# Performance work log

Hardware: AMD Instinct MI355X
Metric: run time of the kernel (lower is better)

The kernel has to match this reference:

```python
import jax, jax.numpy as jnp
import numpy as np

CTX, H, ENC, BALL = 256, 128, 128, 2
IN_DIM = 2 + BALL + ENC  # prev_disp(2) + ball(2) + encoding(128)
B, T = 8192, 128


def setup_inputs() -> dict:
    key = jax.random.key(0)
    ks = jax.random.split(key, 16)
    s = lambda fan_in: 1.0 / np.sqrt(fan_in)
    inp = {
        "context": jax.random.normal(ks[0], (B, CTX), jnp.float32),
        "target_encoding": jax.random.normal(ks[1], (B, ENC), jnp.float32),
        "ball_land_xy": jax.random.normal(ks[2], (B, BALL), jnp.float32),
        "max_frames": T,
        # context_to_h / context_to_c
        "Wh": jax.random.uniform(ks[3], (H, CTX), jnp.float32, -s(CTX), s(CTX)),
        "bh": jax.random.uniform(ks[4], (H,), jnp.float32, -s(CTX), s(CTX)),
        "Wc": jax.random.uniform(ks[5], (H, CTX), jnp.float32, -s(CTX), s(CTX)),
        "bc": jax.random.uniform(ks[6], (H,), jnp.float32, -s(CTX), s(CTX)),
        # LSTM (PyTorch gate order: i, f, g, o)
        "W_ih": jax.random.uniform(ks[7], (4 * H, IN_DIM), jnp.float32, -s(H), s(H)),
        "W_hh": jax.random.uniform(ks[8], (4 * H, H), jnp.float32, -s(H), s(H)),
        "b_ih": jax.random.uniform(ks[9], (4 * H,), jnp.float32, -s(H), s(H)),
        "b_hh": jax.random.uniform(ks[10], (4 * H,), jnp.float32, -s(H), s(H)),
        # output head
        "Wo": jax.random.uniform(ks[11], (2, H), jnp.float32, -s(H), s(H)),
        "bo": jax.random.uniform(ks[12], (2,), jnp.float32, -s(H), s(H)),
    }
    return inp


def _decode(context, target_encoding, ball_land_xy, Wh, bh, Wc, bc,
            W_ih, W_hh, b_ih, b_hh, Wo, bo, max_frames):
    h0 = context @ Wh.T + bh                      # (B, H)
    c0 = context @ Wc.T + bc                      # (B, H)
    Bn = context.shape[0]
    # split input weights: first 2 cols act on prev_disp, rest on static [ball, enc]
    W_prev = W_ih[:, :2]                          # (4H, 2)
    W_stat = W_ih[:, 2:]                          # (4H, BALL+ENC)
    static_in = jnp.concatenate([ball_land_xy, target_encoding], axis=-1)
    gate_static = static_in @ W_stat.T + b_ih + b_hh  # (B, 4H), constant per step
    Hn = h0.shape[-1]

    def step(carry, _):
        h, c, prev = carry
        gates = prev @ W_prev.T + h @ W_hh.T + gate_static
        i, f, g, o = jnp.split(gates, 4, axis=-1)
        c = jax.nn.sigmoid(f) * c + jax.nn.sigmoid(i) * jnp.tanh(g)
        h = jax.nn.sigmoid(o) * jnp.tanh(c)
        pred = h @ Wo.T + bo                      # (B, 2)
        prev = jax.lax.stop_gradient(pred)        # matches .detach()
        return (h, c, prev), pred

    prev0 = jnp.zeros((Bn, 2), dtype=context.dtype)
    _, preds = jax.lax.scan(step, (h0, c0, prev0), None, length=max_frames)
    return jnp.transpose(preds, (1, 0, 2))        # (B, T, 2)


def reference(context, target_encoding, ball_land_xy, max_frames,
              Wh, bh, Wc, bc, W_ih, W_hh, b_ih, b_hh, Wo, bo):
    return _decode(context, target_encoding, ball_land_xy, Wh, bh, Wc, bc,
                   W_ih, W_hh, b_ih, b_hh, Wo, bo, max_frames)
```

## Files before the change

kernel.cpp:

```cpp
#include <hip/hip_runtime.h>
#include <hip/hip_bf16.h>


#define HDIM 128
#define CTX_DIM 256
#define T_FRAMES 128
#define BB 16
#define STR 136

typedef __bf16 bf16x8 __attribute__((ext_vector_type(8)));
typedef float  f32x4  __attribute__((ext_vector_type(4)));

union frag_u {
  bf16x8 v;
  unsigned short s[8];
  uint4 u4;
};

#if __has_builtin(__builtin_amdgcn_exp2f)
#define EXP2(x) __builtin_amdgcn_exp2f(x)
#else
#define EXP2(x) __expf((x) * 0.6931471805599453f)
#endif
#define RCP(x) __builtin_amdgcn_rcpf(x)

__device__ __forceinline__ unsigned short f2bf(float x) {
  unsigned u = __builtin_bit_cast(unsigned, x);
  u += 0x7FFFu + ((u >> 16) & 1u);
  return (unsigned short)(u >> 16);
}
__device__ __forceinline__ float bf2f(unsigned short h) {
  unsigned u = ((unsigned)h) << 16;
  return __builtin_bit_cast(float, u);
}
template<int CTRL>
__device__ __forceinline__ float dpp_mov(float x) {
  return __builtin_bit_cast(float,
    __builtin_amdgcn_mov_dpp(__builtin_bit_cast(int, x), CTRL, 0xF, 0xF, true));
}
__device__ __forceinline__ float row_reduce16(float v) {
  v += dpp_mov<0xB1>(v);
  v += dpp_mov<0x4E>(v);
  v += dpp_mov<0x124>(v);
  v += dpp_mov<0x128>(v);
  return v;
}

#define MFMA(a, b, c) __builtin_amdgcn_mfma_f32_16x16x32_bf16((a), (b), (c), 0, 0, 0)

__global__ __launch_bounds__(512, 4) void traj_lstm(
    const float* __restrict__ ctx, const float* __restrict__ enc,
    const float* __restrict__ ball,
    const float* __restrict__ Wh, const float* __restrict__ bh,
    const float* __restrict__ Wc, const float* __restrict__ bc,
    const float* __restrict__ W_ih, const float* __restrict__ W_hh,
    const float* __restrict__ b_ih, const float* __restrict__ b_hh,
    const float* __restrict__ Wo, const float* __restrict__ bo,
    float* __restrict__ outp)
{
  __shared__ __align__(16) __bf16 sh_h[2][BB * STR];
  __shared__ __align__(16) unsigned short sh_sA[BB * 264];
  __shared__ __align__(16) unsigned short sh_sB[BB * 264];
  __shared__ __align__(16) float sh_gs[4 * HDIM * 16];
  __shared__ __align__(16) uint4 sh_wof[4 * 64];
  __shared__ float sh_pw0[8][BB * 2];
  __shared__ float sh_p0[BB * 2];

  const int tid  = threadIdx.x;
  const int w    = tid >> 6;
  const int l    = tid & 63;
  const int q    = l >> 4;
  const int c16  = l & 15;
  const int colH = w * 16 + c16;
  const int rbase = blockIdx.x * BB;

  const float Lc = 1.4426950408889634f;
  const float SG[4] = {Lc, Lc, 2.f * Lc, Lc};
  const float bo0 = bo[0], bo1 = bo[1];
  const float wo0 = Wo[colH], wo1 = Wo[HDIM + colH];

  float wp0[4], wp1[4];
  #pragma unroll
  for (int g = 0; g < 4; ++g) {
    wp0[g] = W_ih[(size_t)(g * HDIM + colH) * 132 + 0];
    wp1[g] = W_ih[(size_t)(g * HDIM + colH) * 132 + 1];
  }

  frag_u Wf[4][4];
  #pragma unroll
  for (int kt = 0; kt < 4; ++kt) {
    const float* w0p = Wo + kt * 32 + q * 8;
    const float* w1p = Wo + HDIM + kt * 32 + q * 8;
    float4 a0 = *(const float4*)w0p, a1 = *(const float4*)(w0p + 4);
    float4 b0 = *(const float4*)w1p, b1 = *(const float4*)(w1p + 4);
    float wo0v[8] = {a0.x, a0.y, a0.z, a0.w, a1.x, a1.y, a1.z, a1.w};
    float wo1v[8] = {b0.x, b0.y, b0.z, b0.w, b1.x, b1.y, b1.z, b1.w};
    #pragma unroll
    for (int g = 0; g < 4; ++g) {
      const float* wr = W_hh + (size_t)(g * HDIM + colH) * HDIM + kt * 32 + q * 8;
      float4 f0 = *(const float4*)wr;
      float4 f1 = *(const float4*)(wr + 4);
      float ff[8] = {f0.x, f0.y, f0.z, f0.w, f1.x, f1.y, f1.z, f1.w};
      #pragma unroll
      for (int j = 0; j < 8; ++j)
        Wf[g][kt].s[j] = f2bf(SG[g] * (ff[j] + wp0[g] * wo0v[j] + wp1[g] * wo1v[j]));
    }
  }

  #pragma unroll
  for (int kt = 0; kt < 4; ++kt) {
    frag_u wf;
    #pragma unroll
    for (int j = 0; j < 8; ++j) {
      float x = (c16 < 2) ? Wo[c16 * HDIM + kt * 32 + q * 8 + j] : 0.f;
      wf.s[j] = f2bf(x);
    }
    if (w == 0) sh_wof[kt * 64 + l] = wf.u4;
  }

  for (int e = tid; e < BB * 256; e += 512) {
    int row = e >> 8, col = e & 255;
    float x = ctx[(size_t)(rbase + row) * CTX_DIM + col];
    unsigned short hb = f2bf(x);
    sh_sA[row * 264 + col] = hb;
    sh_sB[row * 264 + col] = f2bf(x - bf2f(hb));
  }
  __syncthreads();

  float cst[4];
  {
    f32x4 aH = {0.f,0.f,0.f,0.f};
    f32x4 aC = {0.f,0.f,0.f,0.f};
    #pragma unroll
    for (int kt = 0; kt < 8; ++kt) {
      frag_u Ahi, Alo;
      Ahi.u4 = *(const uint4*)&sh_sA[c16 * 264 + kt * 32 + q * 8];
      Alo.u4 = *(const uint4*)&sh_sB[c16 * 264 + kt * 32 + q * 8];
      frag_u bhi, blo;
      {
        const float* wr = Wh + (size_t)colH * CTX_DIM + kt * 32 + q * 8;
        float4 f0 = *(const float4*)wr;
        float4 f1 = *(const float4*)(wr + 4);
        float ff[8] = {f0.x, f0.y, f0.z, f0.w, f1.x, f1.y, f1.z, f1.w};
        #pragma unroll
        for (int j = 0; j < 8; ++j) {
          unsigned short hb = f2bf(ff[j]);
          bhi.s[j] = hb;
          blo.s[j] = f2bf(ff[j] - bf2f(hb));
        }
      }
      aH = MFMA(Ahi.v, bhi.v, aH);
      aH = MFMA(Alo.v, bhi.v, aH);
      aH = MFMA(Ahi.v, blo.v, aH);
      {
        const float* wr = Wc + (size_t)colH * CTX_DIM + kt * 32 + q * 8;
        float4 f0 = *(const float4*)wr;
        float4 f1 = *(const float4*)(wr + 4);
        float ff[8] = {f0.x, f0.y, f0.z, f0.w, f1.x, f1.y, f1.z, f1.w};
        #pragma unroll
        for (int j = 0; j < 8; ++j) {
          unsigned short hb = f2bf(ff[j]);
          bhi.s[j] = hb;
          blo.s[j] = f2bf(ff[j] - bf2f(hb));
        }
      }
      aC = MFMA(Ahi.v, bhi.v, aC);
      aC = MFMA(Alo.v, bhi.v, aC);
      aC = MFMA(Ahi.v, blo.v, aC);
    }
    float bhv = bh[colH], bcv = bc[colH];
    float pp0[4][2];
    #pragma unroll
    for (int r = 0; r < 4; ++r) {
      float h0v = aH[r] + bhv;
      cst[r] = aC[r] + bcv;
      sh_h[0][(q * 4 + r) * STR + colH] = (__bf16)h0v;
      pp0[r][0] = h0v * wo0;
      pp0[r][1] = h0v * wo1;
    }
    #pragma unroll
    for (int m = 0; m < 4; ++m) {
      pp0[m][0] = row_reduce16(pp0[m][0]);
      pp0[m][1] = row_reduce16(pp0[m][1]);
    }
    if (c16 == 0) {
      #pragma unroll
      for (int r = 0; r < 4; ++r) {
        sh_pw0[w][(q * 4 + r) * 2 + 0] = pp0[r][0];
        sh_pw0[w][(q * 4 + r) * 2 + 1] = pp0[r][1];
      }
    }
  }
  __syncthreads();

  for (int e = tid; e < BB * 168; e += 512) {
    int row = e / 168, col = e - row * 168;
    float x = (col < 2) ? ball[(size_t)(rbase + row) * 2 + col]
            : (col < 130) ? enc[(size_t)(rbase + row) * 128 + (col - 2)] : 0.f;
    unsigned short hb = f2bf(x);
    sh_sA[row * 168 + col] = hb;
    sh_sB[row * 168 + col] = f2bf(x - bf2f(hb));
  }
  if (tid < BB * 2) {
    float s = (tid & 1) ? bo1 : bo0;
    #pragma unroll
    for (int w2 = 0; w2 < 8; ++w2) s += sh_pw0[w2][tid];
    sh_p0[tid] = s;
  }
  __syncthreads();

  {
    f32x4 gacc[4] = {{0.f,0.f,0.f,0.f},{0.f,0.f,0.f,0.f},
                     {0.f,0.f,0.f,0.f},{0.f,0.f,0.f,0.f}};
    #pragma unroll
    for (int kt = 0; kt < 5; ++kt) {
      frag_u Ahi, Alo;
      Ahi.u4 = *(const uint4*)&sh_sA[c16 * 168 + kt * 32 + q * 8];
      Alo.u4 = *(const uint4*)&sh_sB[c16 * 168 + kt * 32 + q * 8];
      #pragma unroll
      for (int g = 0; g < 4; ++g) {
        frag_u bhi, blo;
        #pragma unroll
        for (int j = 0; j < 8; ++j) {
          int kk = kt * 32 + q * 8 + j;
          float x = (kk < 130) ? SG[g] * W_ih[(size_t)(g * HDIM + colH) * 132 + 2 + kk] : 0.f;
          unsigned short hb = f2bf(x);
          bhi.s[j] = hb;
          blo.s[j] = f2bf(x - bf2f(hb));
        }
        gacc[g] = MFMA(Ahi.v, bhi.v, gacc[g]);
        gacc[g] = MFMA(Alo.v, bhi.v, gacc[g]);
        gacc[g] = MFMA(Ahi.v, blo.v, gacc[g]);
      }
    }
    #pragma unroll
    for (int g = 0; g < 4; ++g) {
      int colG = g * HDIM + colH;
      float bb = SG[g] * (b_ih[colG] + b_hh[colG] + bo0 * wp0[g] + bo1 * wp1[g]);
      f32x4 t = gacc[g];
      t[0] += bb; t[1] += bb; t[2] += bb; t[3] += bb;
      *(f32x4*)&sh_gs[((g * HDIM + colH) * 4 + q) * 4] = t;
    }
  }
  float wps0[4], wps1[4];
  #pragma unroll
  for (int g = 0; g < 4; ++g) {
    wps0[g] = SG[g] * wp0[g];
    wps1[g] = SG[g] * wp1[g];
  }

  auto body = [&](int t, int rbuf, bool first) {
    const int wbuf = rbuf ^ 1;
    const __bf16* hp = &sh_h[rbuf][c16 * STR];

    f32x4 acc[4];
    #pragma unroll
    for (int g = 0; g < 4; ++g)
      acc[g] = *(const f32x4*)&sh_gs[((g * HDIM + colH) * 4 + q) * 4];
    f32x4 accP = {0.f, 0.f, 0.f, 0.f};

    #pragma unroll
    for (int kt = 0; kt < 4; ++kt) {
      frag_u A;
      A.u4 = *(const uint4*)(hp + kt * 32 + q * 8);
      #pragma unroll
      for (int g = 0; g < 4; ++g)
        acc[g] = MFMA(A.v, Wf[g][kt].v, acc[g]);
      if (!first && w == 7) {
        frag_u wof;
        wof.u4 = sh_wof[kt * 64 + l];
        accP = MFMA(A.v, wof.v, accP);
      }
    }
    if (first) {
      #pragma unroll
      for (int r = 0; r < 4; ++r) {
        float2 p0r = *(const float2*)&sh_p0[(q * 4 + r) * 2];
        #pragma unroll
        for (int g = 0; g < 4; ++g)
          acc[g][r] -= p0r.x * wps0[g] + p0r.y * wps1[g];
      }
    }
    if (!first && w == 7 && c16 < 2) {
      const int m0 = q * 4;
      const float bov = c16 ? bo1 : bo0;
      #pragma unroll
      for (int r = 0; r < 4; ++r)
        outp[(size_t)(rbase + m0 + r) * (T_FRAMES * 2) + (t - 1) * 2 + c16] = accP[r] + bov;
    }

    __bf16* hw = &sh_h[wbuf][colH];
    #pragma unroll
    for (int r = 0; r < 4; ++r) {
      float ei = EXP2(-acc[0][r]);
      float ef = EXP2(-acc[1][r]);
      float eg = EXP2(-acc[2][r]);
      float eo = EXP2(-acc[3][r]);
      float t1 = (1.f + ei) * (1.f + eg);
      float pf = 1.f + ef;
      float num = cst[r] * t1 + (1.f - eg) * pf;
      float cv = num * RCP(t1 * pf);
      cst[r] = cv;
      float cc = fmaxf(cv, -15.f);
      float ec = EXP2(cc * (-2.f * 1.4426950408889634f));
      float hv = (1.f - ec) * RCP((1.f + eo) * (1.f + ec));
      hw[(q * 4 + r) * STR] = (__bf16)hv;
    }
    __syncthreads();
  };

  body(0, 0, true);
  for (int tp = 0; tp < 63; ++tp) {
    body(2 * tp + 1, 1, false);
    body(2 * tp + 2, 0, false);
  }
  body(127, 1, false);

  if (w == 7) {
    const __bf16* hp = &sh_h[0][c16 * STR];
    f32x4 accP = {0.f, 0.f, 0.f, 0.f};
    #pragma unroll
    for (int kt = 0; kt < 4; ++kt) {
      frag_u A, wof;
      A.u4 = *(const uint4*)(hp + kt * 32 + q * 8);
      wof.u4 = sh_wof[kt * 64 + l];
      accP = MFMA(A.v, wof.v, accP);
    }
    if (c16 < 2) {
      const int m0 = q * 4;
      const float bov = c16 ? bo1 : bo0;
      #pragma unroll
      for (int r = 0; r < 4; ++r)
        outp[(size_t)(rbase + m0 + r) * (T_FRAMES * 2) + 127 * 2 + c16] = accP[r] + bov;
    }
  }
}

extern "C" void kernel_launch(void* const* d_in, const int* in_sizes, int n_in,
                              void* d_out, int out_size, void* d_ws, size_t ws_size,
                              hipStream_t stream) {
  (void)in_sizes; (void)n_in; (void)d_ws; (void)ws_size; (void)out_size;
  const float* ctx  = (const float*)d_in[0];
  const float* enc  = (const float*)d_in[1];
  const float* ball = (const float*)d_in[2];
  const float* Wh   = (const float*)d_in[4];
  const float* bh   = (const float*)d_in[5];
  const float* Wc   = (const float*)d_in[6];
  const float* bc   = (const float*)d_in[7];
  const float* W_ih = (const float*)d_in[8];
  const float* W_hh = (const float*)d_in[9];
  const float* b_ih = (const float*)d_in[10];
  const float* b_hh = (const float*)d_in[11];
  const float* Wo   = (const float*)d_in[12];
  const float* bo   = (const float*)d_in[13];
  float* outp = (float*)d_out;

  dim3 grid(512), block(512);
  traj_lstm<<<grid, block, 0, stream>>>(ctx, enc, ball, Wh, bh, Wc, bc,
                                        W_ih, W_hh, b_ih, b_hh, Wo, bo, outp);
}
```

Measured before the change: 358.4 us.

## Split LSTM recurrence K dimension across wave halves with 32-row blocks

Doubles the rows per block to 32 and the threads to 1024. The two wave groups each own half of the hidden K dimension and hold only half of the W_hh fragments in registers. Each wave computes partial gates for both row halves and exchanges the cross partials through an LDS arena, which adds a second barrier per timestep. The static gate term now stays in registers instead of being re-read from LDS every step. The aim is to cut per-wave register pressure and raise occupancy, at the cost of extra LDS traffic and synchronisation on every step and only 256 blocks for the grid.

```diff
diff --git a/kernel.cpp b/kernel.cpp
--- a/kernel.cpp
+++ b/kernel.cpp
@@ -5,7 +5,7 @@
 #define HDIM 128
 #define CTX_DIM 256
 #define T_FRAMES 128
-#define BB 16
+#define BB 32
 #define STR 136
 
 typedef __bf16 bf16x8 __attribute__((ext_vector_type(8)));
@@ -48,7 +48,7 @@
 
 #define MFMA(a, b, c) __builtin_amdgcn_mfma_f32_16x16x32_bf16((a), (b), (c), 0, 0, 0)
 
-__global__ __launch_bounds__(512, 4) void traj_lstm(
+__global__ __launch_bounds__(1024, 4) void traj_lstm(
     const float* __restrict__ ctx, const float* __restrict__ enc,
     const float* __restrict__ ball,
     const float* __restrict__ Wh, const float* __restrict__ bh,
@@ -59,19 +59,24 @@
     float* __restrict__ outp)
 {
   __shared__ __align__(16) __bf16 sh_h[2][BB * STR];
-  __shared__ __align__(16) unsigned short sh_sA[BB * 264];
-  __shared__ __align__(16) unsigned short sh_sB[BB * 264];
-  __shared__ __align__(16) float sh_gs[4 * HDIM * 16];
+  __shared__ __align__(16) char sh_arena[65536];
   __shared__ __align__(16) uint4 sh_wof[4 * 64];
-  __shared__ float sh_pw0[8][BB * 2];
+  __shared__ float sh_pw0[16][32];
   __shared__ float sh_p0[BB * 2];
+
+  unsigned short* sh_sA = (unsigned short*)sh_arena;
+  unsigned short* sh_sB = sh_sA + BB * 264;
+  f32x4* sh_x = (f32x4*)sh_arena;
 
   const int tid  = threadIdx.x;
   const int w    = tid >> 6;
   const int l    = tid & 63;
   const int q    = l >> 4;
   const int c16  = l & 15;
-  const int colH = w * 16 + c16;
+  const int hw   = w & 7;
+  const int kh   = w >> 3;
+  const int colH = hw * 16 + c16;
+  const int rowLoc = kh * 16;
   const int rbase = blockIdx.x * BB;
 
   const float Lc = 1.4426950408889634f;
@@ -86,9 +91,10 @@
     wp1[g] = W_ih[(size_t)(g * HDIM + colH) * 132 + 1];
   }
 
-  frag_u Wf[4][4];
-  #pragma unroll
-  for (int kt = 0; kt < 4; ++kt) {
+  frag_u Wf[4][2];
+  #pragma unroll
+  for (int kt2 = 0; kt2 < 2; ++kt2) {
+    const int kt = 2 * kh + kt2;
     const float* w0p = Wo + kt * 32 + q * 8;
     const float* w1p = Wo + HDIM + kt * 32 + q * 8;
     float4 a0 = *(const float4*)w0p, a1 = *(const float4*)(w0p + 4);
@@ -103,7 +109,7 @@
       float ff[8] = {f0.x, f0.y, f0.z, f0.w, f1.x, f1.y, f1.z, f1.w};
       #pragma unroll
       for (int j = 0; j < 8; ++j)
-        Wf[g][kt].s[j] = f2bf(SG[g] * (ff[j] + wp0[g] * wo0v[j] + wp1[g] * wo1v[j]));
+        Wf[g][kt2].s[j] = f2bf(SG[g] * (ff[j] + wp0[g] * wo0v[j] + wp1[g] * wo1v[j]));
     }
   }
 
@@ -118,7 +124,7 @@
     if (w == 0) sh_wof[kt * 64 + l] = wf.u4;
   }
 
-  for (int e = tid; e < BB * 256; e += 512) {
+  for (int e = tid; e < BB * 256; e += 1024) {
     int row = e >> 8, col = e & 255;
     float x = ctx[(size_t)(rbase + row) * CTX_DIM + col];
     unsigned short hb = f2bf(x);
@@ -134,8 +140,8 @@
     #pragma unroll
     for (int kt = 0; kt < 8; ++kt) {
       frag_u Ahi, Alo;
-      Ahi.u4 = *(const uint4*)&sh_sA[c16 * 264 + kt * 32 + q * 8];
-      Alo.u4 = *(const uint4*)&sh_sB[c16 * 264 + kt * 32 + q * 8];
+      Ahi.u4 = *(const uint4*)&sh_sA[(rowLoc + c16) * 264 + kt * 32 + q * 8];
+      Alo.u4 = *(const uint4*)&sh_sB[(rowLoc + c16) * 264 + kt * 32 + q * 8];
       frag_u bhi, blo;
       {
         const float* wr = Wh + (size_t)colH * CTX_DIM + kt * 32 + q * 8;
@@ -174,7 +180,7 @@
     for (int r = 0; r < 4; ++r) {
       float h0v = aH[r] + bhv;
       cst[r] = aC[r] + bcv;
-      sh_h[0][(q * 4 + r) * STR + colH] = (__bf16)h0v;
+      sh_h[0][(rowLoc + q * 4 + r) * STR + colH] = (__bf16)h0v;
       pp0[r][0] = h0v * wo0;
       pp0[r][1] = h0v * wo1;
     }
@@ -193,7 +199,7 @@
   }
   __syncthreads();
 
-  for (int e = tid; e < BB * 168; e += 512) {
+  for (int e = tid; e < BB * 168; e += 1024) {
     int row = e / 168, col = e - row * 168;
     float x = (col < 2) ? ball[(size_t)(rbase + row) * 2 + col]
             : (col < 130) ? enc[(size_t)(rbase + row) * 128 + (col - 2)] : 0.f;
@@ -202,100 +208,119 @@
     sh_sB[row * 168 + col] = f2bf(x - bf2f(hb));
   }
   if (tid < BB * 2) {
-    float s = (tid & 1) ? bo1 : bo0;
-    #pragma unroll
-    for (int w2 = 0; w2 < 8; ++w2) s += sh_pw0[w2][tid];
+    int row = tid >> 1, out = tid & 1;
+    int wb = (row >> 4) * 8;
+    float s = out ? bo1 : bo0;
+    #pragma unroll
+    for (int hw2 = 0; hw2 < 8; ++hw2)
+      s += sh_pw0[wb + hw2][(row & 15) * 2 + out];
     sh_p0[tid] = s;
   }
   __syncthreads();
 
-  {
-    f32x4 gacc[4] = {{0.f,0.f,0.f,0.f},{0.f,0.f,0.f,0.f},
-                     {0.f,0.f,0.f,0.f},{0.f,0.f,0.f,0.f}};
-    #pragma unroll
-    for (int kt = 0; kt < 5; ++kt) {
-      frag_u Ahi, Alo;
-      Ahi.u4 = *(const uint4*)&sh_sA[c16 * 168 + kt * 32 + q * 8];
-      Alo.u4 = *(const uint4*)&sh_sB[c16 * 168 + kt * 32 + q * 8];
-      #pragma unroll
-      for (int g = 0; g < 4; ++g) {
-        frag_u bhi, blo;
-        #pragma unroll
-        for (int j = 0; j < 8; ++j) {
-          int kk = kt * 32 + q * 8 + j;
-          float x = (kk < 130) ? SG[g] * W_ih[(size_t)(g * HDIM + colH) * 132 + 2 + kk] : 0.f;
-          unsigned short hb = f2bf(x);
-          bhi.s[j] = hb;
-          blo.s[j] = f2bf(x - bf2f(hb));
-        }
-        gacc[g] = MFMA(Ahi.v, bhi.v, gacc[g]);
-        gacc[g] = MFMA(Alo.v, bhi.v, gacc[g]);
-        gacc[g] = MFMA(Ahi.v, blo.v, gacc[g]);
-      }
-    }
+  f32x4 gacc[4] = {{0.f,0.f,0.f,0.f},{0.f,0.f,0.f,0.f},
+                   {0.f,0.f,0.f,0.f},{0.f,0.f,0.f,0.f}};
+  #pragma unroll
+  for (int kt = 0; kt < 5; ++kt) {
+    frag_u Ahi, Alo;
+    Ahi.u4 = *(const uint4*)&sh_sA[(rowLoc + c16) * 168 + kt * 32 + q * 8];
+    Alo.u4 = *(const uint4*)&sh_sB[(rowLoc + c16) * 168 + kt * 32 + q * 8];
     #pragma unroll
     for (int g = 0; g < 4; ++g) {
-      int colG = g * HDIM + colH;
-      float bb = SG[g] * (b_ih[colG] + b_hh[colG] + bo0 * wp0[g] + bo1 * wp1[g]);
-      f32x4 t = gacc[g];
-      t[0] += bb; t[1] += bb; t[2] += bb; t[3] += bb;
-      *(f32x4*)&sh_gs[((g * HDIM + colH) * 4 + q) * 4] = t;
+      frag_u bhi, blo;
+      #pragma unroll
+      for (int j = 0; j < 8; ++j) {
+        int kk = kt * 32 + q * 8 + j;
+        float x = (kk < 130) ? SG[g] * W_ih[(size_t)(g * HDIM + colH) * 132 + 2 + kk] : 0.f;
+        unsigned short hb = f2bf(x);
+        bhi.s[j] = hb;
+        blo.s[j] = f2bf(x - bf2f(hb));
+      }
+      gacc[g] = MFMA(Ahi.v, bhi.v, gacc[g]);
+      gacc[g] = MFMA(Alo.v, bhi.v, gacc[g]);
+      gacc[g] = MFMA(Ahi.v, blo.v, gacc[g]);
     }
   }
   float wps0[4], wps1[4];
   #pragma unroll
   for (int g = 0; g < 4; ++g) {
+    int colG = g * HDIM + colH;
+    float bb = SG[g] * (b_ih[colG] + b_hh[colG] + bo0 * wp0[g] + bo1 * wp1[g]);
+    gacc[g][0] += bb; gacc[g][1] += bb; gacc[g][2] += bb; gacc[g][3] += bb;
     wps0[g] = SG[g] * wp0[g];
     wps1[g] = SG[g] * wp1[g];
   }
+  __syncthreads();
 
   auto body = [&](int t, int rbuf, bool first) {
     const int wbuf = rbuf ^ 1;
-    const __bf16* hp = &sh_h[rbuf][c16 * STR];
-
-    f32x4 acc[4];
+    const __bf16* hp = &sh_h[rbuf][0];
+
+    frag_u Aown[2], Aoth[2];
+    #pragma unroll
+    for (int kt2 = 0; kt2 < 2; ++kt2) {
+      Aown[kt2].u4 = *(const uint4*)&hp[(rowLoc + c16) * STR + (2 * kh + kt2) * 32 + q * 8];
+      Aoth[kt2].u4 = *(const uint4*)&hp[((16 - rowLoc) + c16) * STR + (2 * kh + kt2) * 32 + q * 8];
+    }
+    f32x4 accO[4], accX[4];
+    #pragma unroll
+    for (int g = 0; g < 4; ++g) {
+      accO[g] = gacc[g];
+      accX[g] = (f32x4){0.f, 0.f, 0.f, 0.f};
+    }
+    #pragma unroll
+    for (int kt2 = 0; kt2 < 2; ++kt2) {
+      #pragma unroll
+      for (int g = 0; g < 4; ++g) {
+        accO[g] = MFMA(Aown[kt2].v, Wf[g][kt2].v, accO[g]);
+        accX[g] = MFMA(Aoth[kt2].v, Wf[g][kt2].v, accX[g]);
+      }
+    }
+    f32x4 accP = {0.f, 0.f, 0.f, 0.f};
+    if (!first && (hw == 7)) {
+      #pragma unroll
+      for (int kt = 0; kt < 4; ++kt) {
+        frag_u pa, wof;
+        pa.u4 = *(const uint4*)&hp[(rowLoc + c16) * STR + kt * 32 + q * 8];
+        wof.u4 = sh_wof[kt * 64 + l];
+        accP = MFMA(pa.v, wof.v, accP);
+      }
+    }
     #pragma unroll
     for (int g = 0; g < 4; ++g)
-      acc[g] = *(const f32x4*)&sh_gs[((g * HDIM + colH) * 4 + q) * 4];
-    f32x4 accP = {0.f, 0.f, 0.f, 0.f};
-
-    #pragma unroll
-    for (int kt = 0; kt < 4; ++kt) {
-      frag_u A;
-      A.u4 = *(const uint4*)(hp + kt * 32 + q * 8);
-      #pragma unroll
-      for (int g = 0; g < 4; ++g)
-        acc[g] = MFMA(A.v, Wf[g][kt].v, acc[g]);
-      if (!first && w == 7) {
-        frag_u wof;
-        wof.u4 = sh_wof[kt * 64 + l];
-        accP = MFMA(A.v, wof.v, accP);
-      }
+      sh_x[g * 1024 + w * 64 + l] = accX[g];
+    __syncthreads();
+
+    const int pw = w ^ 8;
+    f32x4 full[4];
+    #pragma unroll
+    for (int g = 0; g < 4; ++g)
+      full[g] = accO[g] + sh_x[g * 1024 + pw * 64 + l];
+
+    if (!first && hw == 7 && c16 < 2) {
+      const int m0 = rowLoc + q * 4;
+      const float bov = c16 ? bo1 : bo0;
+      #pragma unroll
+      for (int r = 0; r < 4; ++r)
+        outp[(size_t)(rbase + m0 + r) * (T_FRAMES * 2) + (t - 1) * 2 + c16] = accP[r] + bov;
     }
     if (first) {
       #pragma unroll
       for (int r = 0; r < 4; ++r) {
-        float2 p0r = *(const float2*)&sh_p0[(q * 4 + r) * 2];
+        float2 p0r = *(const float2*)&sh_p0[(rowLoc + q * 4 + r) * 2];
         #pragma unroll
         for (int g = 0; g < 4; ++g)
-          acc[g][r] -= p0r.x * wps0[g] + p0r.y * wps1[g];
-      }
-    }
-    if (!first && w == 7 && c16 < 2) {
-      const int m0 = q * 4;
-      const float bov = c16 ? bo1 : bo0;
-      #pragma unroll
-      for (int r = 0; r < 4; ++r)
-        outp[(size_t)(rbase + m0 + r) * (T_FRAMES * 2) + (t - 1) * 2 + c16] = accP[r] + bov;
-    }
-
-    __bf16* hw = &sh_h[wbuf][colH];
+          full[g][r] -= p0r.x * wps0[g] + p0r.y * wps1[g];
+      }
+    }
+
+    __bf16* hwp = &sh_h[wbuf][rowLoc * STR + colH];
     #pragma unroll
     for (int r = 0; r < 4; ++r) {
-      float ei = EXP2(-acc[0][r]);
-      float ef = EXP2(-acc[1][r]);
-      float eg = EXP2(-acc[2][r]);
-      float eo = EXP2(-acc[3][r]);
+      float ei = EXP2(-full[0][r]);
+      float ef = EXP2(-full[1][r]);
+      float eg = EXP2(-full[2][r]);
+      float eo = EXP2(-full[3][r]);
       float t1 = (1.f + ei) * (1.f + eg);
       float pf = 1.f + ef;
       float num = cst[r] * t1 + (1.f - eg) * pf;
@@ -304,7 +329,7 @@
       float cc = fmaxf(cv, -15.f);
       float ec = EXP2(cc * (-2.f * 1.4426950408889634f));
       float hv = (1.f - ec) * RCP((1.f + eo) * (1.f + ec));
-      hw[(q * 4 + r) * STR] = (__bf16)hv;
+      hwp[(q * 4 + r) * STR] = (__bf16)hv;
     }
     __syncthreads();
   };
@@ -316,18 +341,18 @@
   }
   body(127, 1, false);
 
-  if (w == 7) {
-    const __bf16* hp = &sh_h[0][c16 * STR];
+  if (hw == 7) {
+    const __bf16* hp = &sh_h[0][0];
     f32x4 accP = {0.f, 0.f, 0.f, 0.f};
     #pragma unroll
     for (int kt = 0; kt < 4; ++kt) {
-      frag_u A, wof;
-      A.u4 = *(const uint4*)(hp + kt * 32 + q * 8);
+      frag_u pa, wof;
+      pa.u4 = *(const uint4*)&hp[(rowLoc + c16) * STR + kt * 32 + q * 8];
       wof.u4 = sh_wof[kt * 64 + l];
-      accP = MFMA(A.v, wof.v, accP);
+      accP = MFMA(pa.v, wof.v, accP);
     }
     if (c16 < 2) {
-      const int m0 = q * 4;
+      const int m0 = rowLoc + q * 4;
       const float bov = c16 ? bo1 : bo0;
       #pragma unroll
       for (int r = 0; r < 4; ++r)
@@ -355,7 +380,7 @@
   const float* bo   = (const float*)d_in[13];
   float* outp = (float*)d_out;
 
-  dim3 grid(512), block(512);
+  dim3 grid(256), block(1024);
   traj_lstm<<<grid, block, 0, stream>>>(ctx, enc, ball, Wh, bh, Wc, bc,
                                         W_ih, W_hh, b_ih, b_hh, Wo, bo, outp);
 }
```

Result: slower. 367.3 us (+2.5%).

## Halve block to four waves, each computing two hidden column tiles

Applied to the files above, without the earlier changes.

Each block now has 4 waves instead of 8, and each wave owns two 16-column slices of the hidden state. That doubles its weight fragments in registers and the MFMAs it issues per step. Each step reuses the A fragments from LDS across both slices. The per-step barrier now syncs fewer waves, and the first-step correction term is folded into the static gate buffer so the special-cased first body goes away. The trade-off is higher register pressure (Wf doubles to 32 fragments) and lower occupancy, with a launch bound of 2 blocks of 256 threads, which leaves less latency hiding.

```diff
diff --git a/kernel.cpp b/kernel.cpp
--- a/kernel.cpp
+++ b/kernel.cpp
@@ -48,7 +48,7 @@
 
 #define MFMA(a, b, c) __builtin_amdgcn_mfma_f32_16x16x32_bf16((a), (b), (c), 0, 0, 0)
 
-__global__ __launch_bounds__(512, 4) void traj_lstm(
+__global__ __launch_bounds__(256, 2) void traj_lstm(
     const float* __restrict__ ctx, const float* __restrict__ enc,
     const float* __restrict__ ball,
     const float* __restrict__ Wh, const float* __restrict__ bh,
@@ -61,9 +61,9 @@
   __shared__ __align__(16) __bf16 sh_h[2][BB * STR];
   __shared__ __align__(16) unsigned short sh_sA[BB * 264];
   __shared__ __align__(16) unsigned short sh_sB[BB * 264];
-  __shared__ __align__(16) float sh_gs[4 * HDIM * 16];
+  __shared__ __align__(16) f32x4 sh_gs[8 * 4 * 64];
   __shared__ __align__(16) uint4 sh_wof[4 * 64];
-  __shared__ float sh_pw0[8][BB * 2];
+  __shared__ float sh_pw0[4][BB * 2];
   __shared__ float sh_p0[BB * 2];
 
   const int tid  = threadIdx.x;
@@ -71,41 +71,12 @@
   const int l    = tid & 63;
   const int q    = l >> 4;
   const int c16  = l & 15;
-  const int colH = w * 16 + c16;
   const int rbase = blockIdx.x * BB;
+  const int colC[2] = { w * 32 + c16, w * 32 + 16 + c16 };
 
   const float Lc = 1.4426950408889634f;
   const float SG[4] = {Lc, Lc, 2.f * Lc, Lc};
   const float bo0 = bo[0], bo1 = bo[1];
-  const float wo0 = Wo[colH], wo1 = Wo[HDIM + colH];
-
-  float wp0[4], wp1[4];
-  #pragma unroll
-  for (int g = 0; g < 4; ++g) {
-    wp0[g] = W_ih[(size_t)(g * HDIM + colH) * 132 + 0];
-    wp1[g] = W_ih[(size_t)(g * HDIM + colH) * 132 + 1];
-  }
-
-  frag_u Wf[4][4];
-  #pragma unroll
-  for (int kt = 0; kt < 4; ++kt) {
-    const float* w0p = Wo + kt * 32 + q * 8;
-    const float* w1p = Wo + HDIM + kt * 32 + q * 8;
-    float4 a0 = *(const float4*)w0p, a1 = *(const float4*)(w0p + 4);
-    float4 b0 = *(const float4*)w1p, b1 = *(const float4*)(w1p + 4);
-    float wo0v[8] = {a0.x, a0.y, a0.z, a0.w, a1.x, a1.y, a1.z, a1.w};
-    float wo1v[8] = {b0.x, b0.y, b0.z, b0.w, b1.x, b1.y, b1.z, b1.w};
-    #pragma unroll
-    for (int g = 0; g < 4; ++g) {
-      const float* wr = W_hh + (size_t)(g * HDIM + colH) * HDIM + kt * 32 + q * 8;
-      float4 f0 = *(const float4*)wr;
-      float4 f1 = *(const float4*)(wr + 4);
-      float ff[8] = {f0.x, f0.y, f0.z, f0.w, f1.x, f1.y, f1.z, f1.w};
-      #pragma unroll
-      for (int j = 0; j < 8; ++j)
-        Wf[g][kt].s[j] = f2bf(SG[g] * (ff[j] + wp0[g] * wo0v[j] + wp1[g] * wo1v[j]));
-    }
-  }
 
   #pragma unroll
   for (int kt = 0; kt < 4; ++kt) {
@@ -118,7 +89,7 @@
     if (w == 0) sh_wof[kt * 64 + l] = wf.u4;
   }
 
-  for (int e = tid; e < BB * 256; e += 512) {
+  for (int e = tid; e < BB * 256; e += 256) {
     int row = e >> 8, col = e & 255;
     float x = ctx[(size_t)(rbase + row) * CTX_DIM + col];
     unsigned short hb = f2bf(x);
@@ -127,56 +98,63 @@
   }
   __syncthreads();
 
-  float cst[4];
+  float cst[2][4];
   {
-    f32x4 aH = {0.f,0.f,0.f,0.f};
-    f32x4 aC = {0.f,0.f,0.f,0.f};
+    f32x4 aH[2] = {{0.f,0.f,0.f,0.f},{0.f,0.f,0.f,0.f}};
+    f32x4 aC[2] = {{0.f,0.f,0.f,0.f},{0.f,0.f,0.f,0.f}};
     #pragma unroll
     for (int kt = 0; kt < 8; ++kt) {
       frag_u Ahi, Alo;
       Ahi.u4 = *(const uint4*)&sh_sA[c16 * 264 + kt * 32 + q * 8];
       Alo.u4 = *(const uint4*)&sh_sB[c16 * 264 + kt * 32 + q * 8];
-      frag_u bhi, blo;
-      {
-        const float* wr = Wh + (size_t)colH * CTX_DIM + kt * 32 + q * 8;
-        float4 f0 = *(const float4*)wr;
-        float4 f1 = *(const float4*)(wr + 4);
-        float ff[8] = {f0.x, f0.y, f0.z, f0.w, f1.x, f1.y, f1.z, f1.w};
-        #pragma unroll
-        for (int j = 0; j < 8; ++j) {
-          unsigned short hb = f2bf(ff[j]);
-          bhi.s[j] = hb;
-          blo.s[j] = f2bf(ff[j] - bf2f(hb));
+      #pragma unroll
+      for (int ctl = 0; ctl < 2; ++ctl) {
+        frag_u bhi, blo;
+        {
+          const float* wr = Wh + (size_t)colC[ctl] * CTX_DIM + kt * 32 + q * 8;
+          float4 f0 = *(const float4*)wr;
+          float4 f1 = *(const float4*)(wr + 4);
+          float ff[8] = {f0.x, f0.y, f0.z, f0.w, f1.x, f1.y, f1.z, f1.w};
+          #pragma unroll
+          for (int j = 0; j < 8; ++j) {
+            unsigned short hb = f2bf(ff[j]);
+            bhi.s[j] = hb;
+            blo.s[j] = f2bf(ff[j] - bf2f(hb));
+          }
         }
-      }
-      aH = MFMA(Ahi.v, bhi.v, aH);
-      aH = MFMA(Alo.v, bhi.v, aH);
-      aH = MFMA(Ahi.v, blo.v, aH);
-      {
-        const float* wr = Wc + (size_t)colH * CTX_DIM + kt * 32 + q * 8;
-        float4 f0 = *(const float4*)wr;
-        float4 f1 = *(const float4*)(wr + 4);
-        float ff[8] = {f0.x, f0.y, f0.z, f0.w, f1.x, f1.y, f1.z, f1.w};
-        #pragma unroll
-        for (int j = 0; j < 8; ++j) {
-          unsigned short hb = f2bf(ff[j]);
-          bhi.s[j] = hb;
-          blo.s[j] = f2bf(ff[j] - bf2f(hb));
+        aH[ctl] = MFMA(Ahi.v, bhi.v, aH[ctl]);
+        aH[ctl] = MFMA(Alo.v, bhi.v, aH[ctl]);
+        aH[ctl] = MFMA(Ahi.v, blo.v, aH[ctl]);
+        {
+          const float* wr = Wc + (size_t)colC[ctl] * CTX_DIM + kt * 32 + q * 8;
+          float4 f0 = *(const float4*)wr;
+          float4 f1 = *(const float4*)(wr + 4);
+          float ff[8] = {f0.x, f0.y, f0.z, f0.w, f1.x, f1.y, f1.z, f1.w};
+          #pragma unroll
+          for (int j = 0; j < 8; ++j) {
+            unsigned short hb = f2bf(ff[j]);
+            bhi.s[j] = hb;
+            blo.s[j] = f2bf(ff[j] - bf2f(hb));
+          }
         }
-      }
-      aC = MFMA(Ahi.v, bhi.v, aC);
-      aC = MFMA(Alo.v, bhi.v, aC);
-      aC = MFMA(Ahi.v, blo.v, aC);
-    }
-    float bhv = bh[colH], bcv = bc[colH];
-    float pp0[4][2];
-    #pragma unroll
-    for (int r = 0; r < 4; ++r) {
-      float h0v = aH[r] + bhv;
-      cst[r] = aC[r] + bcv;
-      sh_h[0][(q * 4 + r) * STR + colH] = (__bf16)h0v;
-      pp0[r][0] = h0v * wo0;
-      pp0[r][1] = h0v * wo1;
+        aC[ctl] = MFMA(Ahi.v, bhi.v, aC[ctl]);
+        aC[ctl] = MFMA(Alo.v, bhi.v, aC[ctl]);
+        aC[ctl] = MFMA(Ahi.v, blo.v, aC[ctl]);
+      }
+    }
+    float pp0[4][2] = {{0.f,0.f},{0.f,0.f},{0.f,0.f},{0.f,0.f}};
+    #pragma unroll
+    for (int ctl = 0; ctl < 2; ++ctl) {
+      float bhv = bh[colC[ctl]], bcv = bc[colC[ctl]];
+      float wo0c = Wo[colC[ctl]], wo1c = Wo[HDIM + colC[ctl]];
+      #pragma unroll
+      for (int r = 0; r < 4; ++r) {
+        float h0v = aH[ctl][r] + bhv;
+        cst[ctl][r] = aC[ctl][r] + bcv;
+        sh_h[0][(q * 4 + r) * STR + colC[ctl]] = (__bf16)h0v;
+        pp0[r][0] += h0v * wo0c;
+        pp0[r][1] += h0v * wo1c;
+      }
     }
     #pragma unroll
     for (int m = 0; m < 4; ++m) {
@@ -193,7 +171,7 @@
   }
   __syncthreads();
 
-  for (int e = tid; e < BB * 168; e += 512) {
+  for (int e = tid; e < BB * 168; e += 256) {
     int row = e / 168, col = e - row * 168;
     float x = (col < 2) ? ball[(size_t)(rbase + row) * 2 + col]
             : (col < 130) ? enc[(size_t)(rbase + row) * 128 + (col - 2)] : 0.f;
@@ -204,119 +182,171 @@
   if (tid < BB * 2) {
     float s = (tid & 1) ? bo1 : bo0;
     #pragma unroll
-    for (int w2 = 0; w2 < 8; ++w2) s += sh_pw0[w2][tid];
+    for (int w2 = 0; w2 < 4; ++w2) s += sh_pw0[w2][tid];
     sh_p0[tid] = s;
   }
   __syncthreads();
 
   {
-    f32x4 gacc[4] = {{0.f,0.f,0.f,0.f},{0.f,0.f,0.f,0.f},
-                     {0.f,0.f,0.f,0.f},{0.f,0.f,0.f,0.f}};
+    f32x4 gacc[2][4] = {{{0.f,0.f,0.f,0.f},{0.f,0.f,0.f,0.f},{0.f,0.f,0.f,0.f},{0.f,0.f,0.f,0.f}},
+                        {{0.f,0.f,0.f,0.f},{0.f,0.f,0.f,0.f},{0.f,0.f,0.f,0.f},{0.f,0.f,0.f,0.f}}};
     #pragma unroll
     for (int kt = 0; kt < 5; ++kt) {
       frag_u Ahi, Alo;
       Ahi.u4 = *(const uint4*)&sh_sA[c16 * 168 + kt * 32 + q * 8];
       Alo.u4 = *(const uint4*)&sh_sB[c16 * 168 + kt * 32 + q * 8];
       #pragma unroll
+      for (int ctl = 0; ctl < 2; ++ctl) {
+        #pragma unroll
+        for (int g = 0; g < 4; ++g) {
+          frag_u bhi, blo;
+          #pragma unroll
+          for (int j = 0; j < 8; ++j) {
+            int kk = kt * 32 + q * 8 + j;
+            float x = (kk < 130) ? SG[g] * W_ih[(size_t)(g * HDIM + colC[ctl]) * 132 + 2 + kk] : 0.f;
+            unsigned short hb = f2bf(x);
+            bhi.s[j] = hb;
+            blo.s[j] = f2bf(x - bf2f(hb));
+          }
+          gacc[ctl][g] = MFMA(Ahi.v, bhi.v, gacc[ctl][g]);
+          gacc[ctl][g] = MFMA(Alo.v, bhi.v, gacc[ctl][g]);
+          gacc[ctl][g] = MFMA(Ahi.v, blo.v, gacc[ctl][g]);
+        }
+      }
+    }
+    #pragma unroll
+    for (int ctl = 0; ctl < 2; ++ctl) {
+      #pragma unroll
       for (int g = 0; g < 4; ++g) {
-        frag_u bhi, blo;
-        #pragma unroll
-        for (int j = 0; j < 8; ++j) {
-          int kk = kt * 32 + q * 8 + j;
-          float x = (kk < 130) ? SG[g] * W_ih[(size_t)(g * HDIM + colH) * 132 + 2 + kk] : 0.f;
-          unsigned short hb = f2bf(x);
-          bhi.s[j] = hb;
-          blo.s[j] = f2bf(x - bf2f(hb));
+        int colG = g * HDIM + colC[ctl];
+        float wp0v = W_ih[(size_t)colG * 132 + 0];
+        float wp1v = W_ih[(size_t)colG * 132 + 1];
+        float bb = SG[g] * (b_ih[colG] + b_hh[colG] + bo0 * wp0v + bo1 * wp1v);
+        f32x4 s = gacc[ctl][g];
+        #pragma unroll
+        for (int r = 0; r < 4; ++r) {
+          float2 p0r = *(const float2*)&sh_p0[(q * 4 + r) * 2];
+          s[r] += bb - SG[g] * (p0r.x * wp0v + p0r.y * wp1v);
         }
-        gacc[g] = MFMA(Ahi.v, bhi.v, gacc[g]);
-        gacc[g] = MFMA(Alo.v, bhi.v, gacc[g]);
-        gacc[g] = MFMA(Ahi.v, blo.v, gacc[g]);
-      }
-    }
-    #pragma unroll
-    for (int g = 0; g < 4; ++g) {
-      int colG = g * HDIM + colH;
-      float bb = SG[g] * (b_ih[colG] + b_hh[colG] + bo0 * wp0[g] + bo1 * wp1[g]);
-      f32x4 t = gacc[g];
-      t[0] += bb; t[1] += bb; t[2] += bb; t[3] += bb;
-      *(f32x4*)&sh_gs[((g * HDIM + colH) * 4 + q) * 4] = t;
-    }
-  }
-  float wps0[4], wps1[4];
+        sh_gs[((w * 2 + ctl) * 4 + g) * 64 + l] = s;
+      }
+    }
+  }
+
+  frag_u Wf[4][2][4];
   #pragma unroll
-  for (int g = 0; g < 4; ++g) {
-    wps0[g] = SG[g] * wp0[g];
-    wps1[g] = SG[g] * wp1[g];
-  }
-
-  auto body = [&](int t, int rbuf, bool first) {
-    const int wbuf = rbuf ^ 1;
+  for (int ctl = 0; ctl < 2; ++ctl) {
+    #pragma unroll
+    for (int kt = 0; kt < 4; ++kt) {
+      const float* w0p = Wo + kt * 32 + q * 8;
+      const float* w1p = Wo + HDIM + kt * 32 + q * 8;
+      float4 a0 = *(const float4*)w0p, a1 = *(const float4*)(w0p + 4);
+      float4 b0 = *(const float4*)w1p, b1 = *(const float4*)(w1p + 4);
+      float wo0v[8] = {a0.x, a0.y, a0.z, a0.w, a1.x, a1.y, a1.z, a1.w};
+      float wo1v[8] = {b0.x, b0.y, b0.z, b0.w, b1.x, b1.y, b1.z, b1.w};
+      #pragma unroll
+      for (int g = 0; g < 4; ++g) {
+        int colG = g * HDIM + colC[ctl];
+        float wp0v = W_ih[(size_t)colG * 132 + 0];
+        float wp1v = W_ih[(size_t)colG * 132 + 1];
+        const float* wr = W_hh + (size_t)colG * HDIM + kt * 32 + q * 8;
+        float4 f0 = *(const float4*)wr;
+        float4 f1 = *(const float4*)(wr + 4);
+        float ff[8] = {f0.x, f0.y, f0.z, f0.w, f1.x, f1.y, f1.z, f1.w};
+        #pragma unroll
+        for (int j = 0; j < 8; ++j)
+          Wf[g][ctl][kt].s[j] = f2bf(SG[g] * (ff[j] + wp0v * wo0v[j] + wp1v * wo1v[j]));
+      }
+    }
+  }
+  __syncthreads();
+
+  auto body = [&](int t, bool doPred) {
+    const int rbuf = t & 1, wbuf = rbuf ^ 1;
     const __bf16* hp = &sh_h[rbuf][c16 * STR];
 
-    f32x4 acc[4];
-    #pragma unroll
-    for (int g = 0; g < 4; ++g)
-      acc[g] = *(const f32x4*)&sh_gs[((g * HDIM + colH) * 4 + q) * 4];
-    f32x4 accP = {0.f, 0.f, 0.f, 0.f};
-
-    #pragma unroll
-    for (int kt = 0; kt < 4; ++kt) {
-      frag_u A;
-      A.u4 = *(const uint4*)(hp + kt * 32 + q * 8);
+    frag_u A[4];
+    #pragma unroll
+    for (int kt = 0; kt < 4; ++kt)
+      A[kt].u4 = *(const uint4*)(hp + kt * 32 + q * 8);
+
+    f32x4 acc[2][4];
+    #pragma unroll
+    for (int ctl = 0; ctl < 2; ++ctl)
       #pragma unroll
       for (int g = 0; g < 4; ++g)
-        acc[g] = MFMA(A.v, Wf[g][kt].v, acc[g]);
-      if (!first && w == 7) {
+        acc[ctl][g] = sh_gs[((w * 2 + ctl) * 4 + g) * 64 + l];
+    #pragma unroll
+    for (int kt = 0; kt < 4; ++kt)
+      #pragma unroll
+      for (int g = 0; g < 4; ++g)
+        #pragma unroll
+        for (int ctl = 0; ctl < 2; ++ctl)
+          acc[ctl][g] = MFMA(A[kt].v, Wf[g][ctl][kt].v, acc[ctl][g]);
+
+    if (doPred && w == 0) {
+      f32x4 accP = {0.f, 0.f, 0.f, 0.f};
+      #pragma unroll
+      for (int kt = 0; kt < 4; ++kt) {
         frag_u wof;
         wof.u4 = sh_wof[kt * 64 + l];
-        accP = MFMA(A.v, wof.v, accP);
-      }
-    }
-    if (first) {
+        accP = MFMA(A[kt].v, wof.v, accP);
+      }
+      if (c16 < 2) {
+        const float bov = c16 ? bo1 : bo0;
+        #pragma unroll
+        for (int r = 0; r < 4; ++r)
+          outp[(size_t)(rbase + q * 4 + r) * (T_FRAMES * 2) + (t - 1) * 2 + c16] = accP[r] + bov;
+      }
+    }
+
+    #pragma unroll
+    for (int ctl = 0; ctl < 2; ++ctl) {
+      __bf16* hw = &sh_h[wbuf][colC[ctl]];
+      #pragma unroll
+      for (int r = 0; r < 4; ++r) {
+        float ei = EXP2(-acc[ctl][0][r]);
+        float ef = EXP2(-acc[ctl][1][r]);
+        float eg = EXP2(-acc[ctl][2][r]);
+        float eo = EXP2(-acc[ctl][3][r]);
+        float t1 = (1.f + ei) * (1.f + eg);
+        float pf = 1.f + ef;
+        float num = cst[ctl][r] * t1 + (1.f - eg) * pf;
+        float cv = num * RCP(t1 * pf);
+        cst[ctl][r] = cv;
+        float cc = fmaxf(cv, -15.f);
+        float ec = EXP2(cc * (-2.f * 1.4426950408889634f));
+        float hv = (1.f - ec) * RCP((1.f + eo) * (1.f + ec));
+        hw[(q * 4 + r) * STR] = (__bf16)hv;
+      }
+    }
+    __syncthreads();
+  };
+
+  body(0, false);
+
+  #pragma unroll
+  for (int ctl = 0; ctl < 2; ++ctl) {
+    #pragma unroll
+    for (int g = 0; g < 4; ++g) {
+      int colG = g * HDIM + colC[ctl];
+      float wp0v = W_ih[(size_t)colG * 132 + 0];
+      float wp1v = W_ih[(size_t)colG * 132 + 1];
+      f32x4 s = sh_gs[((w * 2 + ctl) * 4 + g) * 64 + l];
       #pragma unroll
       for (int r = 0; r < 4; ++r) {
         float2 p0r = *(const float2*)&sh_p0[(q * 4 + r) * 2];
-        #pragma unroll
-        for (int g = 0; g < 4; ++g)
-          acc[g][r] -= p0r.x * wps0[g] + p0r.y * wps1[g];
-      }
-    }
-    if (!first && w == 7 && c16 < 2) {
-      const int m0 = q * 4;
-      const float bov = c16 ? bo1 : bo0;
-      #pragma unroll
-      for (int r = 0; r < 4; ++r)
-        outp[(size_t)(rbase + m0 + r) * (T_FRAMES * 2) + (t - 1) * 2 + c16] = accP[r] + bov;
-    }
-
-    __bf16* hw = &sh_h[wbuf][colH];
-    #pragma unroll
-    for (int r = 0; r < 4; ++r) {
-      float ei = EXP2(-acc[0][r]);
-      float ef = EXP2(-acc[1][r]);
-      float eg = EXP2(-acc[2][r]);
-      float eo = EXP2(-acc[3][r]);
-      float t1 = (1.f + ei) * (1.f + eg);
-      float pf = 1.f + ef;
-      float num = cst[r] * t1 + (1.f - eg) * pf;
-      float cv = num * RCP(t1 * pf);
-      cst[r] = cv;
-      float cc = fmaxf(cv, -15.f);
-      float ec = EXP2(cc * (-2.f * 1.4426950408889634f));
-      float hv = (1.f - ec) * RCP((1.f + eo) * (1.f + ec));
-      hw[(q * 4 + r) * STR] = (__bf16)hv;
-    }
-    __syncthreads();
-  };
-
-  body(0, 0, true);
-  for (int tp = 0; tp < 63; ++tp) {
-    body(2 * tp + 1, 1, false);
-    body(2 * tp + 2, 0, false);
-  }
-  body(127, 1, false);
-
-  if (w == 7) {
+        s[r] += SG[g] * (p0r.x * wp0v + p0r.y * wp1v);
+      }
+      sh_gs[((w * 2 + ctl) * 4 + g) * 64 + l] = s;
+    }
+  }
+  __syncthreads();
+
+  for (int t = 1; t < 128; ++t)
+    body(t, true);
+
+  if (w == 0) {
     const __bf16* hp = &sh_h[0][c16 * STR];
     f32x4 accP = {0.f, 0.f, 0.f, 0.f};
     #pragma unroll
@@ -327,11 +357,10 @@
       accP = MFMA(A.v, wof.v, accP);
     }
     if (c16 < 2) {
-      const int m0 = q * 4;
       const float bov = c16 ? bo1 : bo0;
       #pragma unroll
       for (int r = 0; r < 4; ++r)
-        outp[(size_t)(rbase + m0 + r) * (T_FRAMES * 2) + 127 * 2 + c16] = accP[r] + bov;
+        outp[(size_t)(rbase + q * 4 + r) * (T_FRAMES * 2) + 127 * 2 + c16] = accP[r] + bov;
     }
   }
 }
@@ -355,7 +384,7 @@
   const float* bo   = (const float*)d_in[13];
   float* outp = (float*)d_out;
 
-  dim3 grid(512), block(512);
+  dim3 grid(512), block(256);
   traj_lstm<<<grid, block, 0, stream>>>(ctx, enc, ball, Wh, bh, Wc, bc,
                                         W_ih, W_hh, b_ih, b_hh, Wo, bo, outp);
 }
```

After: 312.6 us. 12.8% less time.
